# Optimization experiments

Hardware: AMD Instinct MI355X
Metric: run time of the kernel (lower is better)

## Reference

```python
import jax, jax.numpy as jnp
import numpy as np


def setup_inputs() -> dict:
    key = jax.random.key(0)
    k1, k2, k3 = jax.random.split(key, 3)
    B, N, D, T = 8, 2, 256, 500
    SPK = 2000
    H = jax.random.normal(k1, (B, N, D, T), dtype=jnp.float32)
    S = jax.random.randint(k2, (B, N, T), 0, SPK, dtype=jnp.int64)
    E = jax.random.normal(k3, (SPK, D), dtype=jnp.float32)
    alpha = jnp.ones((1,), dtype=jnp.float32) * 10.0
    beta = jnp.ones((1,), dtype=jnp.float32) * 5.0
    return {"H": H, "S": S, "E": E, "alpha": alpha, "beta": beta, "N": 2}


def reference(H, S, E, alpha, beta, N):
    # H: (B, N, D, T); S: (B, N, T) int ids; E: (SPK, D)
    B, N_, D, T = H.shape
    # embedding lookup: (B, N, T, D) -> (B, N, D, T)
    E_S = jnp.transpose(E[S], (0, 1, 3, 2))
    # pairwise dist between predicted vectors and active-speaker embeddings
    # (B, N_pred=N, N_emb=N, T) -- small, direct broadcast
    Dist_p = jnp.sum((H[:, None, :, :, :] - E_S[:, :, None, :, :]) ** 2, axis=3)
    # N == 2 path matching (identity vs swap), min over the two alignments
    p0 = Dist_p[:, 0, 0, :] + Dist_p[:, 1, 1, :]  # (B, T)
    p1 = Dist_p[:, 0, 1, :] + Dist_p[:, 1, 0, :]  # (B, T)
    Dmin = jnp.minimum(p0, p1)                    # (B, T)
    Dmin = -alpha * Dmin + beta                   # broadcast (1,) over (B, T)
    # full distance to every speaker: ||H||^2 + ||E||^2 - 2 H.E
    # avoids materializing (B, SPK, N, D, T)
    Hsq = jnp.sum(H * H, axis=2)                  # (B, N, T)
    Esq = jnp.sum(E * E, axis=1)                  # (SPK,)
    cross = jnp.einsum('bndt,sd->bsnt', H, E)     # (B, SPK, N, T)
    Dist = Hsq[:, None, :, :] + Esq[None, :, None, None] - 2.0 * cross
    Dist = -alpha * Dist + beta                   # (B, SPK, N, T)
    lse = jax.nn.logsumexp(Dist, axis=1)          # (B, N, T)
    loss = -jnp.mean(Dmin) + jnp.mean(lse)
    return (E_S[:, :, :, 0], loss)
```

## Files before the change

### kernel.cpp

```cpp
#include <hip/hip_runtime.h>
#include <math.h>

#define Bb   8
#define Dd   256
#define Tt   500
#define SPK  2000
#define SPKP 2048
#define BN   16
#define L2E  1.4426950408889634f
#define LN2  0.6931471805599453f

#define EXP2F(x) __builtin_amdgcn_exp2f(x)
#define LOG2F(x) __builtin_amdgcn_logf(x)

#define F_ESN   0
#define F_HSQP  4096
#define F_PM    36864
#define F_PL    69632
#define F_DMP2  102400
#define EBF_BYTES ((size_t)167936 * 4)
#define HBF_BYTES (EBF_BYTES + (size_t)1048576)

#define ROWSTRIDE 264
#define BUFELEMS  (64 * ROWSTRIDE)

typedef __bf16 v8bf __attribute__((ext_vector_type(8)));
typedef float  v4f  __attribute__((ext_vector_type(4)));

__device__ inline unsigned pack_bf16x2(float lo, float hi) {
    union { __bf16 h; unsigned short u; } a, b;
    a.h = (__bf16)lo; b.h = (__bf16)hi;
    return ((unsigned)b.u << 16) | (unsigned)a.u;
}

__global__ __launch_bounds__(256) void prep_all_kernel(
        const float* __restrict__ E, const int* __restrict__ S,
        const float* __restrict__ H, const float* __restrict__ alpha,
        const float* __restrict__ beta, float* __restrict__ ws,
        float* __restrict__ out) {
    int bid = blockIdx.x;
    int tid = threadIdx.x;

    if (bid < 512) {
        int s = bid * 4 + (tid >> 6);
        int lane = tid & 63;
        float4 v = make_float4(0.f, 0.f, 0.f, 0.f);
        if (s < SPK) v = ((const float4*)E)[s * 64 + lane];
        __bf16* ebf = (__bf16*)((char*)ws + EBF_BYTES);
        uint2 pp;
        pp.x = pack_bf16x2(v.x, v.y);
        pp.y = pack_bf16x2(v.z, v.w);
        *(uint2*)(ebf + (size_t)s * Dd + lane * 4) = pp;
        float acc = v.x * v.x + v.y * v.y + v.z * v.z + v.w * v.w;
        #pragma unroll
        for (int off = 32; off > 0; off >>= 1) acc += __shfl_down(acc, off, 64);
        if (lane == 0) ws[F_ESN + s] = (s < SPK) ? (-alpha[0] * acc * L2E) : -1e30f;
    } else if (bid < 528) {
        int i = (bid - 512) * 256 + tid;
        int bn = i >> 8, d = i & 255;
        out[i] = E[(size_t)S[bn * Tt] * Dd + d];
    } else {
        __shared__ float trans[32][65];
        int u = bid - 528;
        int bn = u >> 6;
        int r = u & 63;
        int tt0 = (r & 15) * 32;
        int d0 = (r >> 4) * 64;
        const float* Hb = H + (size_t)bn * Dd * Tt;
        #pragma unroll
        for (int p = 0; p < 8; ++p) {
            int flat = p * 256 + tid;
            int dd = flat >> 5;
            int tl = flat & 31;
            int t = tt0 + tl;
            trans[tl][dd] = (t < Tt) ? Hb[(size_t)(d0 + dd) * Tt + t] : 0.f;
        }
        __syncthreads();
        int tw = tid >> 3;
        int j = tid & 7;
        int t = tt0 + tw;
        bool ok = (t < Tt);
        int tc = ok ? t : (Tt - 1);
        int b = bn >> 1;
        int s0 = S[(b * 2 + 0) * Tt + tc];
        int s1 = S[(b * 2 + 1) * Tt + tc];
        const float4* e0p = (const float4*)(E + (size_t)s0 * Dd + d0 + j * 8);
        const float4* e1p = (const float4*)(E + (size_t)s1 * Dd + d0 + j * 8);
        float4 ea0 = e0p[0], ea1 = e0p[1];
        float4 eb0 = e1p[0], eb1 = e1p[1];
        float ev0[8] = {ea0.x, ea0.y, ea0.z, ea0.w, ea1.x, ea1.y, ea1.z, ea1.w};
        float ev1[8] = {eb0.x, eb0.y, eb0.z, eb0.w, eb1.x, eb1.y, eb1.z, eb1.w};
        float sq = 0.f, p0 = 0.f, p1 = 0.f;
        float vals[8];
        #pragma unroll
        for (int e = 0; e < 8; ++e) {
            float x = trans[tw][j * 8 + e];
            vals[e] = x;
            sq = fmaf(x, x, sq);
            float u0 = x - ev0[e]; p0 = fmaf(u0, u0, p0);
            float u1 = x - ev1[e]; p1 = fmaf(u1, u1, p1);
        }
        sq += __shfl_xor(sq, 1, 64); p0 += __shfl_xor(p0, 1, 64); p1 += __shfl_xor(p1, 1, 64);
        sq += __shfl_xor(sq, 2, 64); p0 += __shfl_xor(p0, 2, 64); p1 += __shfl_xor(p1, 2, 64);
        sq += __shfl_xor(sq, 4, 64); p0 += __shfl_xor(p0, 4, 64); p1 += __shfl_xor(p1, 4, 64);
        uint4 pk;
        pk.x = pack_bf16x2(vals[0], vals[1]);
        pk.y = pack_bf16x2(vals[2], vals[3]);
        pk.z = pack_bf16x2(vals[4], vals[5]);
        pk.w = pack_bf16x2(vals[6], vals[7]);
        __bf16* hbf = (__bf16*)((char*)ws + HBF_BYTES);
        *(uint4*)(hbf + ((size_t)(bn * 512 + t) * Dd + d0 + j * 8)) = pk;
        if (j == 0) {
            ws[F_HSQP + (size_t)(bn * 512 + t) * 4 + (r >> 4)] = sq;
            if (ok) {
                float2 pr = make_float2(p0, p1);
                *(float2*)(ws + F_DMP2 + (((size_t)bn * 512 + t) * 4 + (r >> 4)) * 2) = pr;
            }
        }
    }
}

__global__ __launch_bounds__(256, 2) void lse_mfma_kernel(
        const float* __restrict__ alpha, const float* __restrict__ beta,
        float* __restrict__ ws) {
    __shared__ __bf16 shmem[2 * BUFELEMS];
    __shared__ float mrg_m[4][4][16], mrg_l[4][4][16];

    int bn = blockIdx.x;
    int t0 = blockIdx.y * 64;
    int mz = blockIdx.z;
    int tid = threadIdx.x;
    int lane = tid & 63;
    int n = lane & 15;
    int q = lane >> 4;
    int w = tid >> 6;

    const __bf16* ebf = (const __bf16*)((const char*)ws + EBF_BYTES);
    const __bf16* hbf = (const __bf16*)((const char*)ws + HBF_BYTES);

    #pragma unroll
    for (int p = 0; p < 8; ++p) {
        int flat = p * 256 + tid;
        int row = flat >> 5;
        int ch = flat & 31;
        uint4 vb = *(const uint4*)(hbf + ((size_t)(bn * 512 + t0 + row) * Dd + ch * 8));
        uint4 va = *(const uint4*)(ebf + ((size_t)(mz * 512 + row) * Dd + ch * 8));
        *(uint4*)(shmem + row * ROWSTRIDE + ch * 8) = vb;
        *(uint4*)(shmem + BUFELEMS + row * ROWSTRIDE + ch * 8) = va;
    }
    __syncthreads();

    v8bf bq[4][8];
    #pragma unroll
    for (int i = 0; i < 4; ++i) {
        int tloc = 16 * i + n;
        #pragma unroll
        for (int ks = 0; ks < 8; ++ks) {
            bq[i][ks] = *reinterpret_cast<const v8bf*>(&shmem[tloc * ROWSTRIDE + ks * 32 + q * 8]);
        }
    }
    __syncthreads();

    float A = alpha[0], Bv = beta[0];
    float ta2p = 2.f * A * L2E;
    float ctc2[4];
    #pragma unroll
    for (int i = 0; i < 4; ++i) {
        int t = t0 + 16 * i + n;
        float4 hq = *(const float4*)(ws + F_HSQP + (size_t)(bn * 512 + t) * 4);
        float hs = hq.x + hq.y + hq.z + hq.w;
        ctc2[i] = (t < Tt) ? ((Bv - A * hs) * L2E) : 0.f;
    }

    float lm[4], ll[4];
    #pragma unroll
    for (int i = 0; i < 4; ++i) { lm[i] = -INFINITY; ll[i] = 0.f; }

    int curbase = BUFELEMS;
    for (int c = 0; c < 8; ++c) {
        int sbase = mz * 512 + c * 64;
        const __bf16* cb = shmem + curbase;

        v8bf af[8];
        #pragma unroll
        for (int ks = 0; ks < 8; ++ks) {
            af[ks] = *reinterpret_cast<const v8bf*>(&cb[(w * 16 + n) * ROWSTRIDE + ks * 32 + q * 8]);
        }
        float4 es4 = *(const float4*)(ws + F_ESN + sbase + w * 16 + q * 4);

        v4f acc[4];
        #pragma unroll
        for (int i = 0; i < 4; ++i) acc[i] = (v4f){0.f, 0.f, 0.f, 0.f};
        #pragma unroll
        for (int ks = 0; ks < 8; ++ks) {
            #pragma unroll
            for (int i = 0; i < 4; ++i) {
                acc[i] = __builtin_amdgcn_mfma_f32_16x16x32_bf16(af[ks], bq[i][ks], acc[i], 0, 0, 0);
            }
        }
        float e0 = es4.x, e1 = es4.y, e2 = es4.z, e3 = es4.w;
        #pragma unroll
        for (int i = 0; i < 4; ++i) {
            float c2 = ctc2[i];
            float v0 = fmaf(ta2p, acc[i][0], c2 + e0);
            float v1 = fmaf(ta2p, acc[i][1], c2 + e1);
            float v2 = fmaf(ta2p, acc[i][2], c2 + e2);
            float v3 = fmaf(ta2p, acc[i][3], c2 + e3);
            float vm = fmaxf(fmaxf(v0, v1), fmaxf(v2, v3));
            float s = EXP2F(v0 - vm) + EXP2F(v1 - vm) + EXP2F(v2 - vm) + EXP2F(v3 - vm);
            float nm = fmaxf(lm[i], vm);
            ll[i] = ll[i] * EXP2F(lm[i] - nm) + s * EXP2F(vm - nm);
            lm[i] = nm;
        }

        if (c < 7) {
            int nb = sbase + 64;
            __bf16* ob = shmem + (BUFELEMS - curbase);
            #pragma unroll
            for (int p = 0; p < 8; ++p) {
                int flat = p * 256 + tid;
                int row = flat >> 5;
                int ch = flat & 31;
                uint4 v = *(const uint4*)(ebf + ((size_t)(nb + row) * Dd + ch * 8));
                *(uint4*)(ob + row * ROWSTRIDE + ch * 8) = v;
            }
        }
        __syncthreads();
        curbase = BUFELEMS - curbase;
    }

    #pragma unroll
    for (int i = 0; i < 4; ++i) {
        float m = lm[i], l = ll[i];
        #pragma unroll
        for (int msk = 16; msk <= 32; msk <<= 1) {
            float om = __shfl_xor(m, msk, 64);
            float ol = __shfl_xor(l, msk, 64);
            float nm = fmaxf(m, om);
            l = l * EXP2F(m - nm) + ol * EXP2F(om - nm);
            m = nm;
        }
        if (q == 0) { mrg_m[w][i][n] = m; mrg_l[w][i][n] = l; }
    }
    __syncthreads();

    if (tid < 64) {
        int i = tid >> 4, cc = tid & 15;
        float m = mrg_m[0][i][cc], l = mrg_l[0][i][cc];
        #pragma unroll
        for (int wv = 1; wv < 4; ++wv) {
            float om = mrg_m[wv][i][cc], ol = mrg_l[wv][i][cc];
            float nm = fmaxf(m, om);
            l = l * EXP2F(m - nm) + ol * EXP2F(om - nm);
            m = nm;
        }
        int tw = t0 + 16 * i + cc;
        if (tw < Tt) {
            ws[F_PM + (bn * 512 + tw) * 4 + mz] = m;
            ws[F_PL + (bn * 512 + tw) * 4 + mz] = l;
        }
    }
}

__global__ __launch_bounds__(1024) void final_kernel(
        const float* __restrict__ alpha, const float* __restrict__ beta,
        const float* __restrict__ ws, float* __restrict__ out) {
    __shared__ float rL[16], rD[16];
    int tid = threadIdx.x;
    float A = alpha[0], Bv = beta[0];

    float lsum = 0.f;
    #pragma unroll
    for (int it = 0; it < 8; ++it) {
        int idx = it * 1024 + tid;
        int t = idx & 511;
        if (t < Tt) {
            int base = idx * 4;
            float4 m4 = *(const float4*)(ws + F_PM + base);
            float4 l4 = *(const float4*)(ws + F_PL + base);
            float m = m4.x, l = l4.x, nm;
            nm = fmaxf(m, m4.y); l = l * EXP2F(m - nm) + l4.y * EXP2F(m4.y - nm); m = nm;
            nm = fmaxf(m, m4.z); l = l * EXP2F(m - nm) + l4.z * EXP2F(m4.z - nm); m = nm;
            nm = fmaxf(m, m4.w); l = l * EXP2F(m - nm) + l4.w * EXP2F(m4.w - nm); m = nm;
            lsum += LN2 * (m + LOG2F(l));
        }
    }

    float dsum = 0.f;
    #pragma unroll
    for (int it = 0; it < 4; ++it) {
        int idx = it * 1024 + tid;
        int t = idx & 511;
        if (t < Tt) {
            int b = idx >> 9;
            const float4* P0 = (const float4*)(ws + F_DMP2 + ((size_t)(2 * b + 0) * 512 + t) * 8);
            const float4* P1 = (const float4*)(ws + F_DMP2 + ((size_t)(2 * b + 1) * 512 + t) * 8);
            float4 a0 = P0[0], a1 = P0[1];
            float4 b0 = P1[0], b1 = P1[1];
            float d00 = a0.x + a0.z + a1.x + a1.z;
            float d01 = a0.y + a0.w + a1.y + a1.w;
            float d10 = b0.x + b0.z + b1.x + b1.z;
            float d11 = b0.y + b0.w + b1.y + b1.w;
            float dm = fminf(d00 + d11, d01 + d10);
            dsum += -A * dm + Bv;
        }
    }

    int lane = tid & 63, w = tid >> 6;
    #pragma unroll
    for (int off = 32; off > 0; off >>= 1) {
        lsum += __shfl_down(lsum, off, 64);
        dsum += __shfl_down(dsum, off, 64);
    }
    if (lane == 0) { rL[w] = lsum; rD[w] = dsum; }
    __syncthreads();
    if (tid == 0) {
        float L = 0.f, D = 0.f;
        #pragma unroll
        for (int wv = 0; wv < 16; ++wv) { L += rL[wv]; D += rD[wv]; }
        out[BN * Dd] = -(D / (float)(Bb * Tt)) + L / (float)(BN * Tt);
    }
}

extern "C" void kernel_launch(void* const* d_in, const int* in_sizes, int n_in,
                              void* d_out, int out_size, void* d_ws, size_t ws_size,
                              hipStream_t stream) {
    const float* H     = (const float*)d_in[0];
    const int*   S     = (const int*)d_in[1];
    const float* E     = (const float*)d_in[2];
    const float* alpha = (const float*)d_in[3];
    const float* beta  = (const float*)d_in[4];
    float* out = (float*)d_out;
    float* ws  = (float*)d_ws;

    prep_all_kernel<<<1552, 256, 0, stream>>>(E, S, H, alpha, beta, ws, out);
    lse_mfma_kernel<<<dim3(BN, 8, 4), 256, 0, stream>>>(alpha, beta, ws);
    final_kernel<<<1, 1024, 0, stream>>>(alpha, beta, ws, out);
}
```

Measured before the change: 100.2 us.

## Load E fragments directly from global memory and vectorize H transpose loads

The LSE kernel no longer stages E tiles through double-buffered LDS with per-chunk barriers. Each wave now reads its MFMA A-fragments straight from global (L2-resident) memory, and the chunk loop is fully unrolled. This removes the LDS traffic and syncthreads overhead and roughly halves shared memory per block, which may allow higher occupancy. The prep kernel's H transpose also switches to float4 loads. The cost is uncoalesced-ish 16-byte global reads per lane, and the compiler must hide that latency without explicit prefetching.

```diff
diff --git a/kernel.cpp b/kernel.cpp
--- a/kernel.cpp
+++ b/kernel.cpp
@@ -22,7 +22,6 @@
 #define HBF_BYTES (EBF_BYTES + (size_t)1048576)
 
 #define ROWSTRIDE 264
-#define BUFELEMS  (64 * ROWSTRIDE)
 
 typedef __bf16 v8bf __attribute__((ext_vector_type(8)));
 typedef float  v4f  __attribute__((ext_vector_type(4)));
@@ -68,12 +67,25 @@
         int d0 = (r >> 4) * 64;
         const float* Hb = H + (size_t)bn * Dd * Tt;
         #pragma unroll
-        for (int p = 0; p < 8; ++p) {
-            int flat = p * 256 + tid;
-            int dd = flat >> 5;
-            int tl = flat & 31;
-            int t = tt0 + tl;
-            trans[tl][dd] = (t < Tt) ? Hb[(size_t)(d0 + dd) * Tt + t] : 0.f;
+        for (int rep = 0; rep < 2; ++rep) {
+            int pair = rep * 256 + tid;
+            int dd = pair >> 3;
+            int tg = pair & 7;
+            int t = tt0 + tg * 4;
+            const float* src = Hb + (size_t)(d0 + dd) * Tt + t;
+            float4 v;
+            if (t + 3 < Tt) {
+                v = *(const float4*)src;
+            } else {
+                v.x = (t + 0 < Tt) ? src[0] : 0.f;
+                v.y = (t + 1 < Tt) ? src[1] : 0.f;
+                v.z = (t + 2 < Tt) ? src[2] : 0.f;
+                v.w = (t + 3 < Tt) ? src[3] : 0.f;
+            }
+            trans[tg * 4 + 0][dd] = v.x;
+            trans[tg * 4 + 1][dd] = v.y;
+            trans[tg * 4 + 2][dd] = v.z;
+            trans[tg * 4 + 3][dd] = v.w;
         }
         __syncthreads();
         int tw = tid >> 3;
@@ -123,7 +135,7 @@
 __global__ __launch_bounds__(256, 2) void lse_mfma_kernel(
         const float* __restrict__ alpha, const float* __restrict__ beta,
         float* __restrict__ ws) {
-    __shared__ __bf16 shmem[2 * BUFELEMS];
+    __shared__ __bf16 shB[64 * ROWSTRIDE];
     __shared__ float mrg_m[4][4][16], mrg_l[4][4][16];
 
     int bn = blockIdx.x;
@@ -144,9 +156,7 @@
         int row = flat >> 5;
         int ch = flat & 31;
         uint4 vb = *(const uint4*)(hbf + ((size_t)(bn * 512 + t0 + row) * Dd + ch * 8));
-        uint4 va = *(const uint4*)(ebf + ((size_t)(mz * 512 + row) * Dd + ch * 8));
-        *(uint4*)(shmem + row * ROWSTRIDE + ch * 8) = vb;
-        *(uint4*)(shmem + BUFELEMS + row * ROWSTRIDE + ch * 8) = va;
+        *(uint4*)(shB + row * ROWSTRIDE + ch * 8) = vb;
     }
     __syncthreads();
 
@@ -156,10 +166,9 @@
         int tloc = 16 * i + n;
         #pragma unroll
         for (int ks = 0; ks < 8; ++ks) {
-            bq[i][ks] = *reinterpret_cast<const v8bf*>(&shmem[tloc * ROWSTRIDE + ks * 32 + q * 8]);
-        }
-    }
-    __syncthreads();
+            bq[i][ks] = *reinterpret_cast<const v8bf*>(&shB[tloc * ROWSTRIDE + ks * 32 + q * 8]);
+        }
+    }
 
     float A = alpha[0], Bv = beta[0];
     float ta2p = 2.f * A * L2E;
@@ -176,17 +185,17 @@
     #pragma unroll
     for (int i = 0; i < 4; ++i) { lm[i] = -INFINITY; ll[i] = 0.f; }
 
-    int curbase = BUFELEMS;
+    const __bf16* ap = ebf + ((size_t)(mz * 512 + w * 16 + n) * Dd) + q * 8;
+    const float* esb = ws + F_ESN + mz * 512 + w * 16 + q * 4;
+
+    #pragma unroll
     for (int c = 0; c < 8; ++c) {
-        int sbase = mz * 512 + c * 64;
-        const __bf16* cb = shmem + curbase;
-
         v8bf af[8];
         #pragma unroll
         for (int ks = 0; ks < 8; ++ks) {
-            af[ks] = *reinterpret_cast<const v8bf*>(&cb[(w * 16 + n) * ROWSTRIDE + ks * 32 + q * 8]);
-        }
-        float4 es4 = *(const float4*)(ws + F_ESN + sbase + w * 16 + q * 4);
+            af[ks] = *reinterpret_cast<const v8bf*>(ap + (size_t)c * 64 * Dd + ks * 32);
+        }
+        float4 es4 = *(const float4*)(esb + c * 64);
 
         v4f acc[4];
         #pragma unroll
@@ -212,21 +221,6 @@
             ll[i] = ll[i] * EXP2F(lm[i] - nm) + s * EXP2F(vm - nm);
             lm[i] = nm;
         }
-
-        if (c < 7) {
-            int nb = sbase + 64;
-            __bf16* ob = shmem + (BUFELEMS - curbase);
-            #pragma unroll
-            for (int p = 0; p < 8; ++p) {
-                int flat = p * 256 + tid;
-                int row = flat >> 5;
-                int ch = flat & 31;
-                uint4 v = *(const uint4*)(ebf + ((size_t)(nb + row) * Dd + ch * 8));
-                *(uint4*)(ob + row * ROWSTRIDE + ch * 8) = v;
-            }
-        }
-        __syncthreads();
-        curbase = BUFELEMS - curbase;
     }
 
     #pragma unroll
```

Measured after the change: 107.8 us. +7.6%, slower.

## Give each wave private E staging and split final reduction across blocks

Applied to the files above, without the earlier changes.

The MFMA LSE kernel no longer shares a double-buffered 64-row E tile behind block-wide barriers. Each wave now loads its own 16-row E slice from global memory into a private LDS region, waits only on its own LDS writes, and then runs its MFMAs, so the per-chunk __syncthreads disappear. The cost is that global loads are no longer overlapped with compute through double buffering. The final reduction is split across 8 blocks that combine through atomicAdd, with the loss slot zeroed in the prep kernel, which makes the float summation order nondeterministic.

```diff
diff --git a/kernel.cpp b/kernel.cpp
--- a/kernel.cpp
+++ b/kernel.cpp
@@ -22,7 +22,6 @@
 #define HBF_BYTES (EBF_BYTES + (size_t)1048576)
 
 #define ROWSTRIDE 264
-#define BUFELEMS  (64 * ROWSTRIDE)
 
 typedef __bf16 v8bf __attribute__((ext_vector_type(8)));
 typedef float  v4f  __attribute__((ext_vector_type(4)));
@@ -56,6 +55,7 @@
         for (int off = 32; off > 0; off >>= 1) acc += __shfl_down(acc, off, 64);
         if (lane == 0) ws[F_ESN + s] = (s < SPK) ? (-alpha[0] * acc * L2E) : -1e30f;
     } else if (bid < 528) {
+        if (bid == 512 && tid == 0) out[BN * Dd] = 0.f;
         int i = (bid - 512) * 256 + tid;
         int bn = i >> 8, d = i & 255;
         out[i] = E[(size_t)S[bn * Tt] * Dd + d];
@@ -123,7 +123,8 @@
 __global__ __launch_bounds__(256, 2) void lse_mfma_kernel(
         const float* __restrict__ alpha, const float* __restrict__ beta,
         float* __restrict__ ws) {
-    __shared__ __bf16 shmem[2 * BUFELEMS];
+    __shared__ __bf16 shB[64 * ROWSTRIDE];
+    __shared__ __bf16 shA[4 * 16 * ROWSTRIDE];
     __shared__ float mrg_m[4][4][16], mrg_l[4][4][16];
 
     int bn = blockIdx.x;
@@ -144,9 +145,7 @@
         int row = flat >> 5;
         int ch = flat & 31;
         uint4 vb = *(const uint4*)(hbf + ((size_t)(bn * 512 + t0 + row) * Dd + ch * 8));
-        uint4 va = *(const uint4*)(ebf + ((size_t)(mz * 512 + row) * Dd + ch * 8));
-        *(uint4*)(shmem + row * ROWSTRIDE + ch * 8) = vb;
-        *(uint4*)(shmem + BUFELEMS + row * ROWSTRIDE + ch * 8) = va;
+        *(uint4*)(shB + row * ROWSTRIDE + ch * 8) = vb;
     }
     __syncthreads();
 
@@ -156,10 +155,9 @@
         int tloc = 16 * i + n;
         #pragma unroll
         for (int ks = 0; ks < 8; ++ks) {
-            bq[i][ks] = *reinterpret_cast<const v8bf*>(&shmem[tloc * ROWSTRIDE + ks * 32 + q * 8]);
-        }
-    }
-    __syncthreads();
+            bq[i][ks] = *reinterpret_cast<const v8bf*>(&shB[tloc * ROWSTRIDE + ks * 32 + q * 8]);
+        }
+    }
 
     float A = alpha[0], Bv = beta[0];
     float ta2p = 2.f * A * L2E;
@@ -176,17 +174,34 @@
     #pragma unroll
     for (int i = 0; i < 4; ++i) { lm[i] = -INFINITY; ll[i] = 0.f; }
 
-    int curbase = BUFELEMS;
+    __bf16* shAw = shA + w * (16 * ROWSTRIDE);
+
     for (int c = 0; c < 8; ++c) {
-        int sbase = mz * 512 + c * 64;
-        const __bf16* cb = shmem + curbase;
+        int sbase = mz * 512 + c * 64 + w * 16;
+
+        uint4 tmp[8];
+        #pragma unroll
+        for (int p = 0; p < 8; ++p) {
+            int flat = p * 64 + lane;
+            int row = flat >> 5;
+            int ch = flat & 31;
+            tmp[p] = *(const uint4*)(ebf + ((size_t)(sbase + row) * Dd + ch * 8));
+        }
+        #pragma unroll
+        for (int p = 0; p < 8; ++p) {
+            int flat = p * 64 + lane;
+            int row = flat >> 5;
+            int ch = flat & 31;
+            *(uint4*)(shAw + row * ROWSTRIDE + ch * 8) = tmp[p];
+        }
+        __asm__ volatile("s_waitcnt lgkmcnt(0)" ::: "memory");
 
         v8bf af[8];
         #pragma unroll
         for (int ks = 0; ks < 8; ++ks) {
-            af[ks] = *reinterpret_cast<const v8bf*>(&cb[(w * 16 + n) * ROWSTRIDE + ks * 32 + q * 8]);
-        }
-        float4 es4 = *(const float4*)(ws + F_ESN + sbase + w * 16 + q * 4);
+            af[ks] = *reinterpret_cast<const v8bf*>(&shAw[n * ROWSTRIDE + ks * 32 + q * 8]);
+        }
+        float4 es4 = *(const float4*)(ws + F_ESN + sbase - w * 16 + w * 16 + q * 4);
 
         v4f acc[4];
         #pragma unroll
@@ -212,21 +227,6 @@
             ll[i] = ll[i] * EXP2F(lm[i] - nm) + s * EXP2F(vm - nm);
             lm[i] = nm;
         }
-
-        if (c < 7) {
-            int nb = sbase + 64;
-            __bf16* ob = shmem + (BUFELEMS - curbase);
-            #pragma unroll
-            for (int p = 0; p < 8; ++p) {
-                int flat = p * 256 + tid;
-                int row = flat >> 5;
-                int ch = flat & 31;
-                uint4 v = *(const uint4*)(ebf + ((size_t)(nb + row) * Dd + ch * 8));
-                *(uint4*)(ob + row * ROWSTRIDE + ch * 8) = v;
-            }
-        }
-        __syncthreads();
-        curbase = BUFELEMS - curbase;
     }
 
     #pragma unroll
@@ -262,48 +262,38 @@
     }
 }
 
-__global__ __launch_bounds__(1024) void final_kernel(
+__global__ __launch_bounds__(512) void final_kernel(
         const float* __restrict__ alpha, const float* __restrict__ beta,
         const float* __restrict__ ws, float* __restrict__ out) {
-    __shared__ float rL[16], rD[16];
+    __shared__ float rL[8], rD[8];
+    int b = blockIdx.x;
     int tid = threadIdx.x;
     float A = alpha[0], Bv = beta[0];
 
-    float lsum = 0.f;
-    #pragma unroll
-    for (int it = 0; it < 8; ++it) {
-        int idx = it * 1024 + tid;
-        int t = idx & 511;
-        if (t < Tt) {
-            int base = idx * 4;
-            float4 m4 = *(const float4*)(ws + F_PM + base);
-            float4 l4 = *(const float4*)(ws + F_PL + base);
+    float lsum = 0.f, dsum = 0.f;
+    int t = tid;
+    if (t < Tt) {
+        #pragma unroll
+        for (int nn = 0; nn < 2; ++nn) {
+            int idx = (b * 2 + nn) * 512 + t;
+            float4 m4 = *(const float4*)(ws + F_PM + (size_t)idx * 4);
+            float4 l4 = *(const float4*)(ws + F_PL + (size_t)idx * 4);
             float m = m4.x, l = l4.x, nm;
             nm = fmaxf(m, m4.y); l = l * EXP2F(m - nm) + l4.y * EXP2F(m4.y - nm); m = nm;
             nm = fmaxf(m, m4.z); l = l * EXP2F(m - nm) + l4.z * EXP2F(m4.z - nm); m = nm;
             nm = fmaxf(m, m4.w); l = l * EXP2F(m - nm) + l4.w * EXP2F(m4.w - nm); m = nm;
             lsum += LN2 * (m + LOG2F(l));
         }
-    }
-
-    float dsum = 0.f;
-    #pragma unroll
-    for (int it = 0; it < 4; ++it) {
-        int idx = it * 1024 + tid;
-        int t = idx & 511;
-        if (t < Tt) {
-            int b = idx >> 9;
-            const float4* P0 = (const float4*)(ws + F_DMP2 + ((size_t)(2 * b + 0) * 512 + t) * 8);
-            const float4* P1 = (const float4*)(ws + F_DMP2 + ((size_t)(2 * b + 1) * 512 + t) * 8);
-            float4 a0 = P0[0], a1 = P0[1];
-            float4 b0 = P1[0], b1 = P1[1];
-            float d00 = a0.x + a0.z + a1.x + a1.z;
-            float d01 = a0.y + a0.w + a1.y + a1.w;
-            float d10 = b0.x + b0.z + b1.x + b1.z;
-            float d11 = b0.y + b0.w + b1.y + b1.w;
-            float dm = fminf(d00 + d11, d01 + d10);
-            dsum += -A * dm + Bv;
-        }
+        const float4* P0 = (const float4*)(ws + F_DMP2 + ((size_t)(2 * b + 0) * 512 + t) * 8);
+        const float4* P1 = (const float4*)(ws + F_DMP2 + ((size_t)(2 * b + 1) * 512 + t) * 8);
+        float4 a0 = P0[0], a1 = P0[1];
+        float4 b0 = P1[0], b1 = P1[1];
+        float d00 = a0.x + a0.z + a1.x + a1.z;
+        float d01 = a0.y + a0.w + a1.y + a1.w;
+        float d10 = b0.x + b0.z + b1.x + b1.z;
+        float d11 = b0.y + b0.w + b1.y + b1.w;
+        float dm = fminf(d00 + d11, d01 + d10);
+        dsum = -A * dm + Bv;
     }
 
     int lane = tid & 63, w = tid >> 6;
@@ -317,8 +307,8 @@
     if (tid == 0) {
         float L = 0.f, D = 0.f;
         #pragma unroll
-        for (int wv = 0; wv < 16; ++wv) { L += rL[wv]; D += rD[wv]; }
-        out[BN * Dd] = -(D / (float)(Bb * Tt)) + L / (float)(BN * Tt);
+        for (int wv = 0; wv < 8; ++wv) { L += rL[wv]; D += rD[wv]; }
+        atomicAdd(&out[BN * Dd], -(D / (float)(Bb * Tt)) + L / (float)(BN * Tt));
     }
 }
 
@@ -335,5 +325,5 @@
 
     prep_all_kernel<<<1552, 256, 0, stream>>>(E, S, H, alpha, beta, ws, out);
     lse_mfma_kernel<<<dim3(BN, 8, 4), 256, 0, stream>>>(alpha, beta, ws);
-    final_kernel<<<1, 1024, 0, stream>>>(alpha, beta, ws, out);
-}
+    final_kernel<<<8, 512, 0, stream>>>(alpha, beta, ws, out);
+}
```

New measurement: 93.20 us. 7.0% less time.
